# Kernel tuning notes

Hardware: AMD Instinct MI355X
Metric: run time of the kernel (lower is better)

## Reference

```python
import jax, jax.numpy as jnp
import numpy as np

V, T, D, L, H, F = 32000, 1024, 768, 8, 12, 3072
DH = D // H
SCALE = 1.0 / np.sqrt(DH)
EPS = 1e-5


def layer_norm(x, w, b):
    mu = jnp.mean(x, axis=-1, keepdims=True)
    var = jnp.mean(jnp.square(x - mu), axis=-1, keepdims=True)
    return (x - mu) * jax.lax.rsqrt(var + EPS) * w + b


def setup_inputs() -> dict:
    key = jax.random.key(0)
    ks = jax.random.split(key, 10)
    def nrm(k, shape, std=0.02):
        return (jax.random.normal(k, shape, dtype=jnp.float32) * std)
    inp = {
        "idx": jax.random.randint(ks[0], (4, T), 0, V, dtype=jnp.int32),
        "targets": jax.random.randint(ks[1], (4, T), 0, V, dtype=jnp.int32),
        "tok_emb": nrm(ks[2], (V, D)),
        "pos_emb": nrm(ks[3], (T, D)),
        "qkv_w": nrm(ks[4], (L, 3 * D, D)),
        "qkv_b": jnp.zeros((L, 3 * D), jnp.float32),
        "proj_w": nrm(ks[5], (L, D, D)),
        "proj_b": jnp.zeros((L, D), jnp.float32),
        "fc1_w": nrm(ks[6], (L, F, D)),
        "fc1_b": jnp.zeros((L, F), jnp.float32),
        "fc2_w": nrm(ks[7], (L, D, F)),
        "fc2_b": jnp.zeros((L, D), jnp.float32),
        "ln1_w": jnp.ones((L, D), jnp.float32),
        "ln1_b": jnp.zeros((L, D), jnp.float32),
        "ln2_w": jnp.ones((L, D), jnp.float32),
        "ln2_b": jnp.zeros((L, D), jnp.float32),
        "lnf_w": jnp.ones((D,), jnp.float32),
        "lnf_b": jnp.zeros((D,), jnp.float32),
    }
    return inp


def gpt_forward(idx, targets, tok_emb, pos_emb, qkv_w, qkv_b, proj_w, proj_b,
                fc1_w, fc1_b, fc2_w, fc2_b, ln1_w, ln1_b, ln2_w, ln2_b, lnf_w, lnf_b):
    B, Tc = idx.shape
    x = tok_emb[idx] + pos_emb[:Tc][None]  # [B,T,D]
    causal = jnp.tril(jnp.ones((Tc, Tc), bool))

    def block(x, p):
        qw, qb, pw, pb, f1w, f1b, f2w, f2b, l1w, l1b, l2w, l2b = p
        h = layer_norm(x, l1w, l1b)
        qkv = h @ qw.T + qb  # [B,T,3D]
        q, k, v = jnp.split(qkv, 3, axis=-1)
        q = q.reshape(B, Tc, H, DH).transpose(0, 2, 1, 3)  # [B,H,T,DH]
        k = k.reshape(B, Tc, H, DH).transpose(0, 2, 1, 3)
        v = v.reshape(B, Tc, H, DH).transpose(0, 2, 1, 3)
        att = jnp.einsum('bhqd,bhkd->bhqk', q, k) * SCALE
        att = jnp.where(causal, att, -jnp.inf)
        att = jax.nn.softmax(att, axis=-1)
        y = jnp.einsum('bhqk,bhkd->bhqd', att, v)
        y = y.transpose(0, 2, 1, 3).reshape(B, Tc, D)
        x = x + y @ pw.T + pb
        h2 = layer_norm(x, l2w, l2b)
        x = x + jax.nn.gelu(h2 @ f1w.T + f1b, approximate=False) @ f2w.T + f2b
        return x, None

    x, _ = jax.lax.scan(block, x, (qkv_w, qkv_b, proj_w, proj_b,
                                   fc1_w, fc1_b, fc2_w, fc2_b,
                                   ln1_w, ln1_b, ln2_w, ln2_b))
    x = layer_norm(x, lnf_w, lnf_b)
    logits = jnp.einsum('btd,vd->btv', x, tok_emb)  # tied lm_head, output_mult=1
    logp = jax.nn.log_softmax(logits, axis=-1)
    valid = targets != -100
    tgt = jnp.where(valid, targets, 0)
    nll = -jnp.take_along_axis(logp, tgt[..., None], axis=-1)[..., 0]
    loss = jnp.sum(nll * valid) / jnp.maximum(jnp.sum(valid), 1)
    return logits, loss


def reference(idx, targets, tok_emb, pos_emb, qkv_w, qkv_b, proj_w, proj_b,
              fc1_w, fc1_b, fc2_w, fc2_b, ln1_w, ln1_b, ln2_w, ln2_b, lnf_w, lnf_b):
    return gpt_forward(idx, targets, tok_emb, pos_emb, qkv_w, qkv_b, proj_w, proj_b,
                       fc1_w, fc1_b, fc2_w, fc2_b, ln1_w, ln1_b, ln2_w, ln2_b, lnf_w, lnf_b)
```

## Files before the change

kernel.cpp:

```cpp
#include <hip/hip_runtime.h>
#include <hip/hip_bf16.h>
#include <math.h>

#define BATCH 4
#define T 1024
#define D 768
#define L 8
#define H 12
#define F 3072
#define V 32000
#define DH 64
#define M (BATCH*T)
#define D3 (3*D)
#define SCALE 0.125f
#define VCHUNK 6400
#define PBT 125

typedef unsigned short u16;
typedef __attribute__((ext_vector_type(8))) short bf16x8;
typedef __attribute__((ext_vector_type(4))) float f32x4;

__device__ inline u16 f2b(float f) {
  __hip_bfloat16 h = __float2bfloat16(f);
  return *(u16*)&h;
}

__device__ inline void gll16(const void* g, void* l) {
  __builtin_amdgcn_global_load_lds(
      (const __attribute__((address_space(1))) unsigned int*)g,
      (__attribute__((address_space(3))) unsigned int*)l, 16, 0, 0);
}

__device__ inline int swzi(int r, int c) {
  return (r * 64 + c) ^ ((((r & 7) ^ ((r >> 3) & 7))) << 3);
}

__device__ inline float block_reduce(float v, bool is_max, float* buf4) {
  int lane = threadIdx.x & 63, wid = threadIdx.x >> 6;
#pragma unroll
  for (int off = 32; off; off >>= 1) {
    float o = __shfl_down(v, off, 64);
    v = is_max ? fmaxf(v, o) : v + o;
  }
  if (lane == 0) buf4[wid] = v;
  __syncthreads();
  float r = is_max ? fmaxf(fmaxf(buf4[0], buf4[1]), fmaxf(buf4[2], buf4[3]))
                   : buf4[0] + buf4[1] + buf4[2] + buf4[3];
  __syncthreads();
  return r;
}

__global__ __launch_bounds__(256) void k_embed(const int* __restrict__ idx,
                                               const float* __restrict__ tok,
                                               const float* __restrict__ pos,
                                               float* __restrict__ x) {
  int i = blockIdx.x * 256 + threadIdx.x;
  int row = i / D, d = i - row * D;
  int t = row & (T - 1);
  x[i] = tok[(size_t)idx[row] * D + d] + pos[(size_t)t * D + d];
}

__global__ __launch_bounds__(256) void k_cvt(const float* __restrict__ in,
                                             u16* __restrict__ out, int n4) {
  int i = blockIdx.x * 256 + threadIdx.x;
  if (i >= n4) return;
  float4 v = ((const float4*)in)[i];
  ushort4 o;
  o.x = f2b(v.x); o.y = f2b(v.y); o.z = f2b(v.z); o.w = f2b(v.w);
  ((ushort4*)out)[i] = o;
}

__global__ __launch_bounds__(256) void k_cvtw(const float* __restrict__ q,
                                              const float* __restrict__ p,
                                              const float* __restrict__ f1,
                                              const float* __restrict__ f2,
                                              u16* __restrict__ out) {
  const int N0 = L * D3 * D / 4, N1 = L * D * D / 4;
  const int N2 = L * F * D / 4, N3 = L * D * F / 4;
  int i = blockIdx.x * 256 + threadIdx.x;
  if (i >= N0 + N1 + N2 + N3) return;
  const float* src;
  int j = i;
  if (i < N0) { src = q; }
  else if (i < N0 + N1) { src = p; j = i - N0; }
  else if (i < N0 + N1 + N2) { src = f1; j = i - N0 - N1; }
  else { src = f2; j = i - N0 - N1 - N2; }
  float4 v = ((const float4*)src)[j];
  ushort4 o;
  o.x = f2b(v.x); o.y = f2b(v.y); o.z = f2b(v.z); o.w = f2b(v.w);
  ((ushort4*)out)[i] = o;
}

__global__ __launch_bounds__(256) void k_lnorm(const float* __restrict__ x,
                                               const float* __restrict__ w,
                                               const float* __restrict__ b,
                                               u16* __restrict__ out) {
  int lane = threadIdx.x & 63, wid = threadIdx.x >> 6;
  int row = blockIdx.x * 4 + wid;
  const float4* xr = (const float4*)(x + (size_t)row * D);
  float4 v[3];
  float s = 0.f, ss = 0.f;
#pragma unroll
  for (int p = 0; p < 3; ++p) {
    v[p] = xr[lane + 64 * p];
    s += v[p].x + v[p].y + v[p].z + v[p].w;
    ss += v[p].x * v[p].x + v[p].y * v[p].y + v[p].z * v[p].z + v[p].w * v[p].w;
  }
#pragma unroll
  for (int off = 32; off; off >>= 1) {
    s += __shfl_xor(s, off, 64);
    ss += __shfl_xor(ss, off, 64);
  }
  float mu = s * (1.0f / D);
  float var = ss * (1.0f / D) - mu * mu;
  float rs = rsqrtf(var + 1e-5f);
  ushort4* orow = (ushort4*)(out + (size_t)row * D);
#pragma unroll
  for (int p = 0; p < 3; ++p) {
    float4 wv = ((const float4*)w)[lane + 64 * p];
    float4 bv = ((const float4*)b)[lane + 64 * p];
    ushort4 o;
    o.x = f2b((v[p].x - mu) * rs * wv.x + bv.x);
    o.y = f2b((v[p].y - mu) * rs * wv.y + bv.y);
    o.z = f2b((v[p].z - mu) * rs * wv.z + bv.z);
    o.w = f2b((v[p].w - mu) * rs * wv.w + bv.w);
    orow[lane + 64 * p] = o;
  }
}

__global__ __launch_bounds__(512, 2) void k_gemm8(
    const u16* __restrict__ A, const u16* __restrict__ W,
    const float* __restrict__ bias, const float* __restrict__ resid,
    void* __restrict__ Cout, int K, int ldC, int flags) {
  __shared__ __attribute__((aligned(16))) u16 lds[2][2][128 * 64];
  int tid = threadIdx.x, w = tid >> 6, lane = tid & 63;
  int wm = w >> 2, wn = w & 3;
  int bn = blockIdx.x, bm = blockIdx.y;
  int frow = lane & 15, g = lane >> 4;
  int sr = lane >> 3, scu = lane & 7;
  const u16* Ab = A + (size_t)bm * 128 * K;
  const u16* Wb = W + (size_t)bn * 128 * K;
  int NT = K >> 6;

  f32x4 acc[4][2];
#pragma unroll
  for (int i = 0; i < 4; ++i)
#pragma unroll
    for (int j = 0; j < 2; ++j) acc[i][j] = (f32x4)(0.f);

#define STG(t)                                                            \
  {                                                                       \
    _Pragma("unroll") for (int rr = 0; rr < 2; ++rr) {                    \
      int row = rr * 64 + w * 8 + sr;                                     \
      int gcu = scu ^ (row & 7);                                          \
      gll16(Ab + (size_t)row * K + (t) * 64 + gcu * 8,                    \
            &lds[(t) & 1][0][(rr * 64 + w * 8) * 64]);                    \
      gll16(Wb + (size_t)row * K + (t) * 64 + gcu * 8,                    \
            &lds[(t) & 1][1][(rr * 64 + w * 8) * 64]);                    \
    }                                                                     \
  }

  STG(0);
  asm volatile("s_waitcnt vmcnt(0)");
  __builtin_amdgcn_s_barrier();

  for (int t = 0; t < NT; ++t) {
    if (t + 1 < NT) {
      STG(t + 1);
      asm volatile("s_waitcnt vmcnt(4)");
    } else {
      asm volatile("s_waitcnt vmcnt(0)");
    }
    __builtin_amdgcn_s_barrier();
    const u16* bA = &lds[t & 1][0][0];
    const u16* bB = &lds[t & 1][1][0];
    bf16x8 ar[8], br[4];
#pragma unroll
    for (int i = 0; i < 4; ++i)
#pragma unroll
      for (int kk = 0; kk < 2; ++kk) {
        int r = wm * 64 + i * 16 + frow;
        ar[i * 2 + kk] = *(const bf16x8*)(bA + r * 64 + ((g + kk * 4) ^ (r & 7)) * 8);
      }
#pragma unroll
    for (int j = 0; j < 2; ++j)
#pragma unroll
      for (int kk = 0; kk < 2; ++kk) {
        int r = wn * 32 + j * 16 + frow;
        br[j * 2 + kk] = *(const bf16x8*)(bB + r * 64 + ((g + kk * 4) ^ (r & 7)) * 8);
      }
    __builtin_amdgcn_s_setprio(1);
#pragma unroll
    for (int i = 0; i < 4; ++i)
#pragma unroll
      for (int j = 0; j < 2; ++j)
#pragma unroll
        for (int kk = 0; kk < 2; ++kk)
          acc[i][j] = __builtin_amdgcn_mfma_f32_16x16x32_bf16(
              ar[i * 2 + kk], br[j * 2 + kk], acc[i][j], 0, 0, 0);
    __builtin_amdgcn_s_setprio(0);
    __builtin_amdgcn_s_barrier();
  }
#undef STG

  int m0 = bm * 128 + wm * 64 + g * 4;
  int n0 = bn * 128 + wn * 32 + frow;
#pragma unroll
  for (int i = 0; i < 4; ++i) {
#pragma unroll
    for (int j = 0; j < 2; ++j) {
      int n = n0 + j * 16;
      float bv = (flags & 1) ? bias[n] : 0.f;
#pragma unroll
      for (int q = 0; q < 4; ++q) {
        int m = m0 + i * 16 + q;
        size_t off = (size_t)m * ldC + n;
        float v = acc[i][j][q] + bv;
        if (flags & 4) v = 0.5f * v * (1.0f + erff(v * 0.70710678118f));
        if (flags & 2) v += resid[off];
        if (flags & 8) ((u16*)Cout)[off] = f2b(v);
        else           ((float*)Cout)[off] = v;
      }
    }
  }
}

__global__ __launch_bounds__(512, 2) void k_lm256(
    const u16* __restrict__ A,
    const u16* __restrict__ B,
    float* __restrict__ C,
    float* __restrict__ pm, float* __restrict__ ps,
    int gc0) {
  __shared__ __attribute__((aligned(16))) u16 lds[2][2][2][128 * 64];
  __shared__ float pml[256][4], psl[256][4];
  const int K = 768, NT = 12;
  int tid = threadIdx.x, w = tid >> 6, lane = tid & 63;
  int wm = w >> 2, wn = w & 3;
  int bm = blockIdx.y, bn = blockIdx.x;
  int frow = lane & 15, g = lane >> 4;
  int sr = lane >> 3, scu = lane & 7;
  const u16* Abase = A + (size_t)bm * 256 * K;
  const u16* Bbase = B + (size_t)bn * 256 * K;

  f32x4 acc[8][4];
#pragma unroll
  for (int i = 0; i < 8; ++i)
#pragma unroll
    for (int j = 0; j < 4; ++j) acc[i][j] = (f32x4)(0.f);

#define STAGE(t, h)                                                       \
  {                                                                       \
    const u16* src = ((h) < 2 ? Abase : Bbase) + (size_t)(((h)&1) * 128) * K; \
    u16* dst = &lds[(t) & 1][(h) >> 1][(h)&1][0];                         \
    _Pragma("unroll") for (int rr = 0; rr < 2; ++rr) {                    \
      int row = rr * 64 + w * 8 + sr;                                     \
      int gcu = scu ^ (row & 7);                                          \
      gll16(src + (size_t)row * K + (t) * 64 + gcu * 8,                   \
            dst + (rr * 64 + w * 8) * 64);                                \
    }                                                                     \
  }

  bf16x8 ar[8], br[8];
#define LDA(T_, ILO)                                                      \
  {                                                                       \
    const u16* base = &lds[(T_)&1][0][wm][0];                             \
    _Pragma("unroll") for (int ii = 0; ii < 4; ++ii)                      \
    _Pragma("unroll") for (int kk = 0; kk < 2; ++kk) {                    \
      int ri = ((ILO) + ii) * 16 + frow;                                  \
      int u = (g + kk * 4) ^ (ri & 7);                                    \
      ar[ii * 2 + kk] = *(const bf16x8*)(base + ri * 64 + u * 8);         \
    }                                                                     \
  }
#define LDB(T_, JLO, BO)                                                  \
  {                                                                       \
    const u16* base = &lds[(T_)&1][1][wn >> 1][0];                        \
    _Pragma("unroll") for (int jj = 0; jj < 2; ++jj)                      \
    _Pragma("unroll") for (int kk = 0; kk < 2; ++kk) {                    \
      int rj = (wn & 1) * 64 + ((JLO) + jj) * 16 + frow;                  \
      int u = (g + kk * 4) ^ (rj & 7);                                    \
      br[(BO) + jj * 2 + kk] = *(const bf16x8*)(base + rj * 64 + u * 8);  \
    }                                                                     \
  }
#define MFMA16(ILO, JLO, BO)                                              \
  _Pragma("unroll") for (int ii = 0; ii < 4; ++ii)                        \
  _Pragma("unroll") for (int jj = 0; jj < 2; ++jj)                        \
  _Pragma("unroll") for (int kk = 0; kk < 2; ++kk)                        \
    acc[(ILO) + ii][(JLO) + jj] = __builtin_amdgcn_mfma_f32_16x16x32_bf16( \
        ar[ii * 2 + kk], br[(BO) + jj * 2 + kk], acc[(ILO) + ii][(JLO) + jj], 0, 0, 0);

  STAGE(0, 0); STAGE(0, 1); STAGE(0, 2); STAGE(0, 3);
  asm volatile("s_waitcnt vmcnt(0)");
  __builtin_amdgcn_s_barrier();

  for (int t = 0; t < NT; ++t) {
    bool pf = (t + 1 < NT);
    LDA(t, 0); LDB(t, 0, 0);
    if (pf) { STAGE(t + 1, 0); STAGE(t + 1, 1); }
    __builtin_amdgcn_s_setprio(1);
    MFMA16(0, 0, 0);
    __builtin_amdgcn_s_setprio(0);
    __builtin_amdgcn_s_barrier();
    LDB(t, 2, 4);
    if (pf) { STAGE(t + 1, 2); STAGE(t + 1, 3); }
    __builtin_amdgcn_s_setprio(1);
    MFMA16(0, 2, 4);
    __builtin_amdgcn_s_setprio(0);
    __builtin_amdgcn_s_barrier();
    LDA(t, 4);
    __builtin_amdgcn_s_setprio(1);
    MFMA16(4, 2, 4);
    __builtin_amdgcn_s_setprio(0);
    __builtin_amdgcn_s_barrier();
    __builtin_amdgcn_s_setprio(1);
    MFMA16(4, 0, 0);
    __builtin_amdgcn_s_setprio(0);
    asm volatile("s_waitcnt vmcnt(0)");
    __builtin_amdgcn_s_barrier();
  }

#pragma unroll
  for (int ii = 0; ii < 8; ++ii) {
#pragma unroll
    for (int q = 0; q < 4; ++q) {
      float mx = fmaxf(fmaxf(acc[ii][0][q], acc[ii][1][q]),
                       fmaxf(acc[ii][2][q], acc[ii][3][q]));
      mx = fmaxf(mx, __shfl_xor(mx, 1, 64));
      mx = fmaxf(mx, __shfl_xor(mx, 2, 64));
      mx = fmaxf(mx, __shfl_xor(mx, 4, 64));
      mx = fmaxf(mx, __shfl_xor(mx, 8, 64));
      float sm = 0.f;
#pragma unroll
      for (int jj = 0; jj < 4; ++jj) sm += __expf(acc[ii][jj][q] - mx);
      sm += __shfl_xor(sm, 1, 64);
      sm += __shfl_xor(sm, 2, 64);
      sm += __shfl_xor(sm, 4, 64);
      sm += __shfl_xor(sm, 8, 64);
      int lrow = wm * 128 + ii * 16 + g * 4 + q;
      if (frow == 0) { pml[lrow][wn] = mx; psl[lrow][wn] = sm; }
      size_t off = (size_t)(bm * 256 + lrow) * V + gc0 + bn * 256 + wn * 64 + frow;
#pragma unroll
      for (int jj = 0; jj < 4; ++jj) C[off + jj * 16] = acc[ii][jj][q];
    }
  }
  __syncthreads();
  if (tid < 256) {
    float m = fmaxf(fmaxf(pml[tid][0], pml[tid][1]), fmaxf(pml[tid][2], pml[tid][3]));
    float s = 0.f;
#pragma unroll
    for (int w4 = 0; w4 < 4; ++w4) s += psl[tid][w4] * __expf(pml[tid][w4] - m);
    size_t grow = bm * 256 + tid;
    int pb = gc0 / 256 + bn;
    pm[grow * PBT + pb] = m;
    ps[grow * PBT + pb] = s;
  }
#undef STAGE
#undef LDA
#undef LDB
#undef MFMA16
}

__global__ __launch_bounds__(256) void k_fattn(const u16* __restrict__ qkv,
                                               u16* __restrict__ y) {
  __shared__ __attribute__((aligned(16))) u16 lQ[128 * 64];
  __shared__ __attribute__((aligned(16))) u16 lK[64 * 64];
  __shared__ __attribute__((aligned(16))) u16 lVt[64 * 64];
  __shared__ __attribute__((aligned(16))) u16 lP[128 * 64];
  int tid = threadIdx.x;
  int w = tid >> 6, lane = tid & 63;
  int qtb = blockIdx.x;
  int bh = blockIdx.y, b = bh / H, h = bh - b * H;
  int q0 = qtb * 128;
  const u16* base = qkv + (size_t)b * T * D3 + h * DH;
  int srow = lane >> 3;
  int scu = lane & 7;
  int frow = lane & 15, g = lane >> 4;
  int w16 = w * 16;
  int qrow = g * 4;

#pragma unroll
  for (int c = 0; c < 4; ++c) {
    int row = c * 32 + w * 8 + srow;
    int gcu = scu ^ (row & 7);
    gll16(base + (size_t)(q0 + row) * D3 + gcu * 8, lQ + (c * 32 + w * 8) * 64);
  }

  float m_r[2][4], l_r[2][4];
  f32x4 o[2][4];
#pragma unroll
  for (int s = 0; s < 2; ++s)
#pragma unroll
    for (int i = 0; i < 4; ++i) {
      m_r[s][i] = -1e30f; l_r[s][i] = 0.f; o[s][i] = (f32x4)(0.f);
    }

  int ktmax = 2 * qtb + 1;
  uint4 kr[2], vr[2];
#pragma unroll
  for (int c = 0; c < 2; ++c) {
    int row = c * 32 + w * 8 + srow;
    kr[c] = *(const uint4*)(base + D + (size_t)row * D3 + scu * 8);
    vr[c] = *(const uint4*)(base + 2 * D + (size_t)row * D3 + scu * 8);
  }

  for (int kt = 0; kt <= ktmax; ++kt) {
    __syncthreads();
    int k0 = kt * 64;
#pragma unroll
    for (int c = 0; c < 2; ++c) {
      int row = c * 32 + w * 8 + srow;
      *(uint4*)(lK + row * 64 + (scu ^ (row & 7)) * 8) = kr[c];
      unsigned vals[4] = {vr[c].x, vr[c].y, vr[c].z, vr[c].w};
#pragma unroll
      for (int e = 0; e < 4; ++e) {
        lVt[swzi(scu * 8 + 2 * e, row)]     = (u16)(vals[e] & 0xffff);
        lVt[swzi(scu * 8 + 2 * e + 1, row)] = (u16)(vals[e] >> 16);
      }
    }
    __syncthreads();
    if (kt < ktmax) {
      int k0n = k0 + 64;
#pragma unroll
      for (int c = 0; c < 2; ++c) {
        int row = c * 32 + w * 8 + srow;
        kr[c] = *(const uint4*)(base + D + (size_t)(k0n + row) * D3 + scu * 8);
        vr[c] = *(const uint4*)(base + 2 * D + (size_t)(k0n + row) * D3 + scu * 8);
      }
    }

#pragma unroll
    for (int s = 0; s < 2; ++s) {
      if (kt > 2 * qtb + s) continue;
      int qs = s * 64 + w16;
      int f7 = frow & 7;
      bf16x8 aq0 = *(const bf16x8*)(lQ + (qs + frow) * 64 + (g ^ f7) * 8);
      bf16x8 aq1 = *(const bf16x8*)(lQ + (qs + frow) * 64 + ((g + 4) ^ f7) * 8);
      f32x4 sv[4];
#pragma unroll
      for (int kn = 0; kn < 4; ++kn) {
        bf16x8 bk0 = *(const bf16x8*)(lK + (kn * 16 + frow) * 64 + (g ^ f7) * 8);
        bf16x8 bk1 = *(const bf16x8*)(lK + (kn * 16 + frow) * 64 + ((g + 4) ^ f7) * 8);
        sv[kn] = __builtin_amdgcn_mfma_f32_16x16x32_bf16(aq0, bk0, (f32x4)(0.f), 0, 0, 0);
        sv[kn] = __builtin_amdgcn_mfma_f32_16x16x32_bf16(aq1, bk1, sv[kn], 0, 0, 0);
      }
#pragma unroll
      for (int kn = 0; kn < 4; ++kn)
#pragma unroll
        for (int qi = 0; qi < 4; ++qi) {
          float v = sv[kn][qi] * SCALE;
          if (kt == 2 * qtb + s) {
            int qg = q0 + qs + qrow + qi;
            int kg = k0 + kn * 16 + frow;
            if (kg > qg) v = -1e30f;
          }
          sv[kn][qi] = v;
        }
#pragma unroll
      for (int qi = 0; qi < 4; ++qi) {
        float rm = fmaxf(fmaxf(sv[0][qi], sv[1][qi]), fmaxf(sv[2][qi], sv[3][qi]));
        rm = fmaxf(rm, __shfl_xor(rm, 1, 64));
        rm = fmaxf(rm, __shfl_xor(rm, 2, 64));
        rm = fmaxf(rm, __shfl_xor(rm, 4, 64));
        rm = fmaxf(rm, __shfl_xor(rm, 8, 64));
        float mn = fmaxf(m_r[s][qi], rm);
        float alpha = __expf(m_r[s][qi] - mn);
        m_r[s][qi] = mn;
        float rs = 0.f;
#pragma unroll
        for (int kn = 0; kn < 4; ++kn) {
          float p = __expf(sv[kn][qi] - mn);
          sv[kn][qi] = p;
          rs += p;
        }
        rs += __shfl_xor(rs, 1, 64);
        rs += __shfl_xor(rs, 2, 64);
        rs += __shfl_xor(rs, 4, 64);
        rs += __shfl_xor(rs, 8, 64);
        l_r[s][qi] = l_r[s][qi] * alpha + rs;
#pragma unroll
        for (int df = 0; df < 4; ++df) o[s][df][qi] *= alpha;
      }
#pragma unroll
      for (int kn = 0; kn < 4; ++kn)
#pragma unroll
        for (int qi = 0; qi < 4; ++qi)
          lP[swzi(qs + qrow + qi, kn * 16 + frow)] = f2b(sv[kn][qi]);
      bf16x8 pa0 = *(const bf16x8*)(lP + swzi(qs + frow, g * 8));
      bf16x8 pa1 = *(const bf16x8*)(lP + swzi(qs + frow, 32 + g * 8));
#pragma unroll
      for (int df = 0; df < 4; ++df) {
        bf16x8 bv0 = *(const bf16x8*)(lVt + swzi(df * 16 + frow, g * 8));
        bf16x8 bv1 = *(const bf16x8*)(lVt + swzi(df * 16 + frow, 32 + g * 8));
        o[s][df] = __builtin_amdgcn_mfma_f32_16x16x32_bf16(pa0, bv0, o[s][df], 0, 0, 0);
        o[s][df] = __builtin_amdgcn_mfma_f32_16x16x32_bf16(pa1, bv1, o[s][df], 0, 0, 0);
      }
    }
  }

#pragma unroll
  for (int s = 0; s < 2; ++s)
#pragma unroll
    for (int df = 0; df < 4; ++df)
#pragma unroll
      for (int qi = 0; qi < 4; ++qi) {
        int qg = q0 + s * 64 + w16 + qrow + qi;
        y[(size_t)(b * T + qg) * D + h * DH + df * 16 + frow] =
            f2b(o[s][df][qi] / l_r[s][qi]);
      }
}

__global__ __launch_bounds__(256) void k_loss_rows(
    const float* __restrict__ pm, const float* __restrict__ ps,
    const float* __restrict__ logits, const int* __restrict__ targets,
    float* __restrict__ nll) {
  int lane = threadIdx.x & 63, wid = threadIdx.x >> 6;
  int row = blockIdx.x * 4 + wid;
  const float* pmr = pm + (size_t)row * PBT;
  const float* psr = ps + (size_t)row * PBT;
  float m = -1e30f;
  for (int i = lane; i < PBT; i += 64) m = fmaxf(m, pmr[i]);
#pragma unroll
  for (int off = 32; off; off >>= 1) m = fmaxf(m, __shfl_xor(m, off, 64));
  float s = 0.f;
  for (int i = lane; i < PBT; i += 64) s += psr[i] * __expf(pmr[i] - m);
#pragma unroll
  for (int off = 32; off; off >>= 1) s += __shfl_xor(s, off, 64);
  if (lane == 0) {
    int tgt = targets[row];
    nll[row] = (tgt != -100) ? (m + logf(s) - logits[(size_t)row * V + tgt]) : 0.f;
  }
}

__global__ __launch_bounds__(256) void k_loss_final(const float* __restrict__ nll,
                                                    const int* __restrict__ targets,
                                                    float* __restrict__ out) {
  __shared__ float buf4[4];
  float s = 0.f, c = 0.f;
  for (int i = threadIdx.x; i < M; i += 256) {
    s += nll[i];
    c += (targets[i] != -100) ? 1.f : 0.f;
  }
  s = block_reduce(s, false, buf4);
  c = block_reduce(c, false, buf4);
  if (threadIdx.x == 0) out[0] = s / fmaxf(c, 1.f);
}

extern "C" void kernel_launch(void* const* d_in, const int* in_sizes, int n_in,
                              void* d_out, int out_size, void* d_ws, size_t ws_size,
                              hipStream_t stream) {
  const int* idx       = (const int*)d_in[0];
  const int* targets   = (const int*)d_in[1];
  const float* tok     = (const float*)d_in[2];
  const float* pos     = (const float*)d_in[3];
  const float* qkv_w   = (const float*)d_in[4];
  const float* qkv_b   = (const float*)d_in[5];
  const float* proj_w  = (const float*)d_in[6];
  const float* proj_b  = (const float*)d_in[7];
  const float* fc1_w   = (const float*)d_in[8];
  const float* fc1_b   = (const float*)d_in[9];
  const float* fc2_w   = (const float*)d_in[10];
  const float* fc2_b   = (const float*)d_in[11];
  const float* ln1_w   = (const float*)d_in[12];
  const float* ln1_b   = (const float*)d_in[13];
  const float* ln2_w   = (const float*)d_in[14];
  const float* ln2_b   = (const float*)d_in[15];
  const float* lnf_w   = (const float*)d_in[16];
  const float* lnf_b   = (const float*)d_in[17];

  float* logits = (float*)d_out;

  char* ws = (char*)d_ws;
  float* x   = (float*)ws;
  u16* hb    = (u16*)(ws + 12582912);
  u16* yb    = (u16*)(ws + 18874368);
  u16* wb    = (u16*)(ws + 25165824);
  float* pm  = (float*)(ws + 34996224);
  float* ps  = (float*)(ws + 37044224);
  float* nll = (float*)(ws + 39092224);

  u16* qkvb   = (u16*)logits;
  u16* f1b    = (u16*)(logits + 9437184);
  u16* wqkv   = (u16*)(logits + 15728640);
  u16* wproj  = (u16*)(logits + 22806528);
  u16* wfc1   = (u16*)(logits + 25165824);
  u16* wfc2   = (u16*)(logits + 34603008);

  {
    const int NW4 = (L * D3 * D + L * D * D + L * F * D + L * D * F) / 4;
    k_cvtw<<<(NW4 + 255) / 256, 256, 0, stream>>>(qkv_w, proj_w, fc1_w, fc2_w, wqkv);
  }

  k_embed<<<(M * D) / 256, 256, 0, stream>>>(idx, tok, pos, x);

  for (int l = 0; l < L; ++l) {
    k_lnorm<<<M / 4, 256, 0, stream>>>(x, ln1_w + (size_t)l * D, ln1_b + (size_t)l * D, hb);
    k_gemm8<<<dim3(D3 / 128, M / 128), 512, 0, stream>>>(
        hb, wqkv + (size_t)l * D3 * D, qkv_b + (size_t)l * D3, nullptr, qkvb, D, D3, 9);
    k_fattn<<<dim3(T / 128, BATCH * H), 256, 0, stream>>>(qkvb, yb);
    k_gemm8<<<dim3(D / 128, M / 128), 512, 0, stream>>>(
        yb, wproj + (size_t)l * D * D, proj_b + (size_t)l * D, x, x, D, D, 3);
    k_lnorm<<<M / 4, 256, 0, stream>>>(x, ln2_w + (size_t)l * D, ln2_b + (size_t)l * D, hb);
    k_gemm8<<<dim3(F / 128, M / 128), 512, 0, stream>>>(
        hb, wfc1 + (size_t)l * F * D, fc1_b + (size_t)l * F, nullptr, f1b, D, F, 13);
    k_gemm8<<<dim3(D / 128, M / 128), 512, 0, stream>>>(
        f1b, wfc2 + (size_t)l * D * F, fc2_b + (size_t)l * D, x, x, F, D, 3);
  }

  k_lnorm<<<M / 4, 256, 0, stream>>>(x, lnf_w, lnf_b, hb);
  for (int c = 0; c < 5; ++c) {
    k_cvt<<<(VCHUNK * D / 4 + 255) / 256, 256, 0, stream>>>(
        tok + (size_t)c * VCHUNK * D, wb, VCHUNK * D / 4);
    k_lm256<<<dim3(VCHUNK / 256, M / 256), 512, 0, stream>>>(
        hb, wb, logits, pm, ps, c * VCHUNK);
  }
  k_loss_rows<<<M / 4, 256, 0, stream>>>(pm, ps, logits, targets, nll);
  k_loss_final<<<1, 256, 0, stream>>>(nll, targets, logits + (size_t)M * V);
}
```

Measured before the change: 2.182 ms.

## Balance causal attention work by pairing early and late query tiles per block

Each attention block now processes two 64-row query tiles, 15-xi and xi, instead of one contiguous 128-row tile. This equalizes the number of causal K/V tiles each block visits, removing the load imbalance where late blocks did far more work. The shared P buffer shrinks, and the diagonal masking is recomputed per tile.

Result: faster. 1.999 ms (-8.4%).

```diff
diff --git a/kernel.cpp b/kernel.cpp
--- a/kernel.cpp
+++ b/kernel.cpp
@@ -361,15 +361,17 @@
 
 __global__ __launch_bounds__(256) void k_fattn(const u16* __restrict__ qkv,
                                                u16* __restrict__ y) {
-  __shared__ __attribute__((aligned(16))) u16 lQ[128 * 64];
+  __shared__ __attribute__((aligned(16))) u16 lQ[2][64 * 64];
   __shared__ __attribute__((aligned(16))) u16 lK[64 * 64];
   __shared__ __attribute__((aligned(16))) u16 lVt[64 * 64];
-  __shared__ __attribute__((aligned(16))) u16 lP[128 * 64];
+  __shared__ __attribute__((aligned(16))) u16 lP[64 * 64];
   int tid = threadIdx.x;
   int w = tid >> 6, lane = tid & 63;
-  int qtb = blockIdx.x;
+  int xi = blockIdx.x;
   int bh = blockIdx.y, b = bh / H, h = bh - b * H;
-  int q0 = qtb * 128;
+  int qt[2];
+  qt[0] = 15 - xi;
+  qt[1] = xi;
   const u16* base = qkv + (size_t)b * T * D3 + h * DH;
   int srow = lane >> 3;
   int scu = lane & 7;
@@ -378,11 +380,14 @@
   int qrow = g * 4;
 
 #pragma unroll
-  for (int c = 0; c < 4; ++c) {
-    int row = c * 32 + w * 8 + srow;
-    int gcu = scu ^ (row & 7);
-    gll16(base + (size_t)(q0 + row) * D3 + gcu * 8, lQ + (c * 32 + w * 8) * 64);
-  }
+  for (int tq = 0; tq < 2; ++tq)
+#pragma unroll
+    for (int c = 0; c < 2; ++c) {
+      int row = c * 32 + w * 8 + srow;
+      int gcu = scu ^ (row & 7);
+      gll16(base + (size_t)(qt[tq] * 64 + row) * D3 + gcu * 8,
+            &lQ[tq][(c * 32 + w * 8) * 64]);
+    }
 
   float m_r[2][4], l_r[2][4];
   f32x4 o[2][4];
@@ -393,7 +398,7 @@
       m_r[s][i] = -1e30f; l_r[s][i] = 0.f; o[s][i] = (f32x4)(0.f);
     }
 
-  int ktmax = 2 * qtb + 1;
+  int ktmax = 15 - xi;
   uint4 kr[2], vr[2];
 #pragma unroll
   for (int c = 0; c < 2; ++c) {
@@ -428,12 +433,14 @@
     }
 
 #pragma unroll
-    for (int s = 0; s < 2; ++s) {
-      if (kt > 2 * qtb + s) continue;
-      int qs = s * 64 + w16;
+    for (int tq = 0; tq < 2; ++tq) {
+      if (tq == 1 && kt > xi) continue;
+      bool diag = (kt == qt[tq]);
+      int qglob0 = qt[tq] * 64 + w16;
       int f7 = frow & 7;
-      bf16x8 aq0 = *(const bf16x8*)(lQ + (qs + frow) * 64 + (g ^ f7) * 8);
-      bf16x8 aq1 = *(const bf16x8*)(lQ + (qs + frow) * 64 + ((g + 4) ^ f7) * 8);
+      const u16* lq = &lQ[tq][0];
+      bf16x8 aq0 = *(const bf16x8*)(lq + (w16 + frow) * 64 + (g ^ f7) * 8);
+      bf16x8 aq1 = *(const bf16x8*)(lq + (w16 + frow) * 64 + ((g + 4) ^ f7) * 8);
       f32x4 sv[4];
 #pragma unroll
       for (int kn = 0; kn < 4; ++kn) {
@@ -447,8 +454,8 @@
 #pragma unroll
         for (int qi = 0; qi < 4; ++qi) {
           float v = sv[kn][qi] * SCALE;
-          if (kt == 2 * qtb + s) {
-            int qg = q0 + qs + qrow + qi;
+          if (diag) {
+            int qg = qglob0 + qrow + qi;
             int kg = k0 + kn * 16 + frow;
             if (kg > qg) v = -1e30f;
           }
@@ -461,9 +468,9 @@
         rm = fmaxf(rm, __shfl_xor(rm, 2, 64));
         rm = fmaxf(rm, __shfl_xor(rm, 4, 64));
         rm = fmaxf(rm, __shfl_xor(rm, 8, 64));
-        float mn = fmaxf(m_r[s][qi], rm);
-        float alpha = __expf(m_r[s][qi] - mn);
-        m_r[s][qi] = mn;
+        float mn = fmaxf(m_r[tq][qi], rm);
+        float alpha = __expf(m_r[tq][qi] - mn);
+        m_r[tq][qi] = mn;
         float rs = 0.f;
 #pragma unroll
         for (int kn = 0; kn < 4; ++kn) {
@@ -475,36 +482,36 @@
         rs += __shfl_xor(rs, 2, 64);
         rs += __shfl_xor(rs, 4, 64);
         rs += __shfl_xor(rs, 8, 64);
-        l_r[s][qi] = l_r[s][qi] * alpha + rs;
-#pragma unroll
-        for (int df = 0; df < 4; ++df) o[s][df][qi] *= alpha;
+        l_r[tq][qi] = l_r[tq][qi] * alpha + rs;
+#pragma unroll
+        for (int df = 0; df < 4; ++df) o[tq][df][qi] *= alpha;
       }
 #pragma unroll
       for (int kn = 0; kn < 4; ++kn)
 #pragma unroll
         for (int qi = 0; qi < 4; ++qi)
-          lP[swzi(qs + qrow + qi, kn * 16 + frow)] = f2b(sv[kn][qi]);
-      bf16x8 pa0 = *(const bf16x8*)(lP + swzi(qs + frow, g * 8));
-      bf16x8 pa1 = *(const bf16x8*)(lP + swzi(qs + frow, 32 + g * 8));
+          lP[swzi(w16 + qrow + qi, kn * 16 + frow)] = f2b(sv[kn][qi]);
+      bf16x8 pa0 = *(const bf16x8*)(lP + swzi(w16 + frow, g * 8));
+      bf16x8 pa1 = *(const bf16x8*)(lP + swzi(w16 + frow, 32 + g * 8));
 #pragma unroll
       for (int df = 0; df < 4; ++df) {
         bf16x8 bv0 = *(const bf16x8*)(lVt + swzi(df * 16 + frow, g * 8));
         bf16x8 bv1 = *(const bf16x8*)(lVt + swzi(df * 16 + frow, 32 + g * 8));
-        o[s][df] = __builtin_amdgcn_mfma_f32_16x16x32_bf16(pa0, bv0, o[s][df], 0, 0, 0);
-        o[s][df] = __builtin_amdgcn_mfma_f32_16x16x32_bf16(pa1, bv1, o[s][df], 0, 0, 0);
-      }
-    }
-  }
-
-#pragma unroll
-  for (int s = 0; s < 2; ++s)
+        o[tq][df] = __builtin_amdgcn_mfma_f32_16x16x32_bf16(pa0, bv0, o[tq][df], 0, 0, 0);
+        o[tq][df] = __builtin_amdgcn_mfma_f32_16x16x32_bf16(pa1, bv1, o[tq][df], 0, 0, 0);
+      }
+    }
+  }
+
+#pragma unroll
+  for (int tq = 0; tq < 2; ++tq)
 #pragma unroll
     for (int df = 0; df < 4; ++df)
 #pragma unroll
       for (int qi = 0; qi < 4; ++qi) {
-        int qg = q0 + s * 64 + w16 + qrow + qi;
+        int qg = qt[tq] * 64 + w16 + qrow + qi;
         y[(size_t)(b * T + qg) * D + h * DH + df * 16 + frow] =
-            f2b(o[s][df][qi] / l_r[s][qi]);
+            f2b(o[tq][df][qi] / l_r[tq][qi]);
       }
 }
 
@@ -595,7 +602,7 @@
     k_lnorm<<<M / 4, 256, 0, stream>>>(x, ln1_w + (size_t)l * D, ln1_b + (size_t)l * D, hb);
     k_gemm8<<<dim3(D3 / 128, M / 128), 512, 0, stream>>>(
         hb, wqkv + (size_t)l * D3 * D, qkv_b + (size_t)l * D3, nullptr, qkvb, D, D3, 9);
-    k_fattn<<<dim3(T / 128, BATCH * H), 256, 0, stream>>>(qkvb, yb);
+    k_fattn<<<dim3(8, BATCH * H), 256, 0, stream>>>(qkvb, yb);
     k_gemm8<<<dim3(D / 128, M / 128), 512, 0, stream>>>(
         yb, wproj + (size_t)l * D * D, proj_b + (size_t)l * D, x, x, D, D, 3);
     k_lnorm<<<M / 4, 256, 0, stream>>>(x, ln2_w + (size_t)l * D, ln2_b + (size_t)l * D, hb);
```
